# Optimization experiments

Hardware: AMD Instinct MI355X
Metric: run time of the kernel (lower is better)

## Reference

```python
import jax, jax.numpy as jnp
import numpy as np


def setup_inputs() -> dict:
    key = jax.random.key(0)
    k1, k2, k3 = jax.random.split(key, 3)
    B, idf, cdf, L, ih, iw = 16, 1024, 256, 256, 64, 64
    M = ih * iw  # 4096, conv_context2 output channels
    # scale inputs so attention logits are O(1) and softmax isn't saturated
    weightedContext = jax.random.normal(k1, (B, idf, M), dtype=jnp.float32) * 0.02
    context = jax.random.normal(k2, (B, cdf, L), dtype=jnp.float32)
    # conv1x1(cdf -> ih*iw) weight, fan-in init scale 1/sqrt(cdf)
    w2 = jax.random.normal(k3, (M, cdf), dtype=jnp.float32) * (1.0 / np.sqrt(cdf))
    return {"weightedContext": weightedContext, "context": context, "w2": w2,
            "ih": ih, "iw": iw}


def reference(weightedContext, context, w2, ih, iw):
    B = context.shape[0]
    idf = weightedContext.shape[1]
    # conv1x1 on [B, cdf, L, 1] == per-position linear: [B, ih*iw, L]
    sourceC = jnp.einsum('mc,bcl->bml', w2, context)
    # attn logits: bmm([B, idf, M], [B, M, L]) -> [B, idf, L]
    attn = jnp.einsum('bim,bml->bil', weightedContext, sourceC)
    # nn.Softmax() on [B*idf, L] view -> softmax over sourceL (last dim)
    attn = jax.nn.softmax(attn, axis=-1)
    # transpose to [B, L, idf]
    attn_c = jnp.transpose(attn, (0, 2, 1))
    # bmm([B, M, L], [B, L, idf]) -> [B, M, idf]
    wc = jnp.einsum('bml,bli->bmi', sourceC, attn_c)
    # transpose -> [B, idf, M] -> [B, idf, ih, iw]
    weightedContext_c = jnp.transpose(wc, (0, 2, 1)).reshape(B, idf, ih, iw)
    return weightedContext_c, attn_c
```

## Files before the change

### kernel.cpp

```cpp
#include <hip/hip_runtime.h>

typedef __bf16 bf16;
typedef __bf16 bf16x4 __attribute__((ext_vector_type(4)));
typedef __bf16 bf16x8 __attribute__((ext_vector_type(8)));
typedef float  f32x4  __attribute__((ext_vector_type(4)));

constexpr int NB  = 16;
constexpr int IDF = 1024;
constexpr int CDF = 256;
constexpr int L   = 256;
constexpr int M   = 4096;

__global__ __launch_bounds__(256) void k_prep_w2(const float* __restrict__ w2,
                                                 bf16* __restrict__ w2b) {
    int i = (blockIdx.x * 256 + threadIdx.x) * 4;
    float4 v = *reinterpret_cast<const float4*>(w2 + i);
    bf16x4 o; o[0] = (bf16)v.x; o[1] = (bf16)v.y; o[2] = (bf16)v.z; o[3] = (bf16)v.w;
    *reinterpret_cast<bf16x4*>(w2b + i) = o;
}

__global__ __launch_bounds__(256) void k_prep_ctxT(const float* __restrict__ ctx,
                                                   bf16* __restrict__ ctxT) {
    __shared__ float tb[32][33];
    int b = blockIdx.z, c0 = blockIdx.y * 32, l0 = blockIdx.x * 32;
    int tx = threadIdx.x, ty = threadIdx.y;
    const float* src = ctx + (size_t)b * CDF * L;
#pragma unroll
    for (int j = 0; j < 4; j++) tb[ty + 8*j][tx] = src[(size_t)(c0 + ty + 8*j) * L + l0 + tx];
    __syncthreads();
    bf16* dst = ctxT + (size_t)b * L * CDF;
#pragma unroll
    for (int j = 0; j < 4; j++) dst[(size_t)(l0 + ty + 8*j) * CDF + c0 + tx] = (bf16)tb[tx][ty + 8*j];
}

__global__ __launch_bounds__(256) void k_gemm1(const bf16* __restrict__ w2b,
                                               const bf16* __restrict__ ctxT,
                                               bf16* __restrict__ SC,
                                               bf16* __restrict__ ST) {
    __shared__ alignas(16) char smem[2 * 128 * 72 * 2];
    bf16 (*As)[72]  = reinterpret_cast<bf16(*)[72]>(smem);
    bf16 (*Bs)[72]  = reinterpret_cast<bf16(*)[72]>(smem + 128 * 72 * 2);
    bf16 (*Cs)[136] = reinterpret_cast<bf16(*)[136]>(smem);

    const int b  = blockIdx.z;
    const int m0 = blockIdx.y * 128;
    const int l0 = blockIdx.x * 128;
    const int t = threadIdx.x;
    const int lane = t & 63, wid = t >> 6;
    const int wr = (wid >> 1) * 64, wc = (wid & 1) * 64;

    const bf16* Ag = w2b + (size_t)m0 * CDF;
    const bf16* Bg = ctxT + (size_t)b * L * CDF + (size_t)l0 * CDF;

    f32x4 acc[4][4] = {};
    for (int k0 = 0; k0 < CDF; k0 += 64) {
#pragma unroll
        for (int j = 0; j < 4; j++) {
            int idx = (j * 256 + t) * 8; int r = idx >> 6, c = idx & 63;
            *reinterpret_cast<bf16x8*>(&As[r][c]) =
                *reinterpret_cast<const bf16x8*>(&Ag[(size_t)r * CDF + k0 + c]);
        }
#pragma unroll
        for (int j = 0; j < 4; j++) {
            int idx = (j * 256 + t) * 8; int r = idx >> 6, c = idx & 63;
            *reinterpret_cast<bf16x8*>(&Bs[r][c]) =
                *reinterpret_cast<const bf16x8*>(&Bg[(size_t)r * CDF + k0 + c]);
        }
        __syncthreads();
#pragma unroll
        for (int kk = 0; kk < 2; kk++) {
            const int kb = kk * 32 + (lane >> 4) * 8;
            bf16x8 af[4], bb[4];
#pragma unroll
            for (int f = 0; f < 4; f++)
                af[f] = *reinterpret_cast<const bf16x8*>(&As[wr + f * 16 + (lane & 15)][kb]);
#pragma unroll
            for (int f = 0; f < 4; f++)
                bb[f] = *reinterpret_cast<const bf16x8*>(&Bs[wc + f * 16 + (lane & 15)][kb]);
#pragma unroll
            for (int fm = 0; fm < 4; fm++)
#pragma unroll
                for (int fn = 0; fn < 4; fn++)
                    acc[fm][fn] = __builtin_amdgcn_mfma_f32_16x16x32_bf16(af[fm], bb[fn], acc[fm][fn], 0, 0, 0);
        }
        __syncthreads();
    }
#pragma unroll
    for (int fm = 0; fm < 4; fm++)
#pragma unroll
        for (int fn = 0; fn < 4; fn++) {
            int row = wr + fm * 16 + ((lane >> 4) << 2);
            int col = wc + fn * 16 + (lane & 15);
#pragma unroll
            for (int r = 0; r < 4; r++) Cs[row + r][col] = (bf16)acc[fm][fn][r];
        }
    __syncthreads();
    bf16* sc = SC + (size_t)b * M * L + (size_t)m0 * L + l0;
#pragma unroll
    for (int j = 0; j < 8; j++) {
        int idx = (j * 256 + t) * 8; int r = idx >> 7, c = idx & 127;
        *reinterpret_cast<bf16x8*>(&sc[(size_t)r * L + c]) =
            *reinterpret_cast<const bf16x8*>(&Cs[r][c]);
    }
    bf16* st = ST + (size_t)b * L * M + (size_t)l0 * M + m0;
#pragma unroll
    for (int j = 0; j < 8; j++) {
        int idx = (j * 256 + t) * 8; int lr = idx >> 7, c = idx & 127;
        bf16x8 v;
#pragma unroll
        for (int u = 0; u < 8; u++) v[u] = Cs[c + u][lr];
        *reinterpret_cast<bf16x8*>(&st[(size_t)lr * M + c]) = v;
    }
}

__global__ __launch_bounds__(256) void k_attn(const float* __restrict__ WC,
                                              const bf16* __restrict__ ST,
                                              bf16* __restrict__ AT,
                                              float* __restrict__ attn_c) {
    __shared__ alignas(16) char smem[32 * 72 * 2 + 256 * 72 * 2];
    bf16 (*As)[72] = reinterpret_cast<bf16(*)[72]>(smem);
    bf16 (*Bs)[72] = reinterpret_cast<bf16(*)[72]>(smem + 32 * 72 * 2);
    float (*Lg)[257] = reinterpret_cast<float(*)[257]>(smem);
    __shared__ float red[32][9];
    __shared__ float invbuf[32];

    const int b  = blockIdx.y;
    const int i0 = blockIdx.x * 32;
    const int t = threadIdx.x;
    const int lane = t & 63, w = t >> 6;

    const float* Ag = WC + (size_t)b * IDF * M + (size_t)i0 * M;
    const bf16*  Bg = ST + (size_t)b * L * M;

    f32x4 acc[2][4] = {};
    for (int k0 = 0; k0 < M; k0 += 64) {
#pragma unroll
        for (int j = 0; j < 2; j++) {
            int idx = (j * 256 + t) * 4; int r = idx >> 6, c = idx & 63;
            float4 v = *reinterpret_cast<const float4*>(&Ag[(size_t)r * M + k0 + c]);
            bf16x4 o; o[0] = (bf16)v.x; o[1] = (bf16)v.y; o[2] = (bf16)v.z; o[3] = (bf16)v.w;
            *reinterpret_cast<bf16x4*>(&As[r][c]) = o;
        }
#pragma unroll
        for (int j = 0; j < 8; j++) {
            int idx = (j * 256 + t) * 8; int r = idx >> 6, c = idx & 63;
            *reinterpret_cast<bf16x8*>(&Bs[r][c]) =
                *reinterpret_cast<const bf16x8*>(&Bg[(size_t)r * M + k0 + c]);
        }
        __syncthreads();
#pragma unroll
        for (int kk = 0; kk < 2; kk++) {
            const int kb = kk * 32 + (lane >> 4) * 8;
            bf16x8 af[2], bb[4];
#pragma unroll
            for (int f = 0; f < 2; f++)
                af[f] = *reinterpret_cast<const bf16x8*>(&As[f * 16 + (lane & 15)][kb]);
#pragma unroll
            for (int f = 0; f < 4; f++)
                bb[f] = *reinterpret_cast<const bf16x8*>(&Bs[w * 64 + f * 16 + (lane & 15)][kb]);
#pragma unroll
            for (int fm = 0; fm < 2; fm++)
#pragma unroll
                for (int fn = 0; fn < 4; fn++)
                    acc[fm][fn] = __builtin_amdgcn_mfma_f32_16x16x32_bf16(af[fm], bb[fn], acc[fm][fn], 0, 0, 0);
        }
        __syncthreads();
    }
#pragma unroll
    for (int fm = 0; fm < 2; fm++)
#pragma unroll
        for (int fn = 0; fn < 4; fn++) {
            int row = fm * 16 + ((lane >> 4) << 2);
            int col = w * 64 + fn * 16 + (lane & 15);
#pragma unroll
            for (int r = 0; r < 4; r++) Lg[row + r][col] = acc[fm][fn][r];
        }
    __syncthreads();
    const int srow = t & 31, sseg = t >> 5;
    float mx = -3.0e38f;
    for (int j = 0; j < 32; j++) mx = fmaxf(mx, Lg[srow][sseg * 32 + j]);
    red[srow][sseg] = mx;
    __syncthreads();
    float mrow = red[srow][0];
#pragma unroll
    for (int s = 1; s < 8; s++) mrow = fmaxf(mrow, red[srow][s]);
    __syncthreads();
    float ps = 0.f;
    for (int j = 0; j < 32; j++) {
        float e = __expf(Lg[srow][sseg * 32 + j] - mrow);
        Lg[srow][sseg * 32 + j] = e;
        ps += e;
    }
    red[srow][sseg] = ps;
    __syncthreads();
    float sum = 0.f;
#pragma unroll
    for (int s = 0; s < 8; s++) sum += red[srow][s];
    const float inv = 1.0f / sum;
    if (sseg == 0) invbuf[srow] = inv;
    __syncthreads();
    bf16* at = AT + (size_t)b * IDF * L + (size_t)i0 * L;
#pragma unroll
    for (int u = 0; u < 4; u++) {
        bf16x8 v;
#pragma unroll
        for (int q = 0; q < 8; q++) v[q] = (bf16)(Lg[srow][sseg * 32 + u * 8 + q] * inv);
        *reinterpret_cast<bf16x8*>(&at[(size_t)srow * L + sseg * 32 + u * 8]) = v;
    }
    float* ac = attn_c + (size_t)b * L * IDF + i0;
    const int i = t & 31, ls = t >> 5;
    const float invi = invbuf[i];
    for (int l = ls; l < L; l += 8)
        ac[(size_t)l * IDF + i] = Lg[i][l] * invi;
}

__global__ __launch_bounds__(256) void k_gemm3(const bf16* __restrict__ AT,
                                               const bf16* __restrict__ SC,
                                               float* __restrict__ out0) {
    __shared__ alignas(16) bf16 As[128][72];
    __shared__ alignas(16) bf16 Bs[128][72];
    const int b  = blockIdx.z;
    const int i0 = blockIdx.y * 128;
    const int m0 = blockIdx.x * 128;
    const int t = threadIdx.x;
    const int lane = t & 63, wid = t >> 6;
    const int wr = (wid >> 1) * 64, wc = (wid & 1) * 64;
    const bf16* Ag = AT + (size_t)b * IDF * L + (size_t)i0 * L;
    const bf16* Bg = SC + (size_t)b * M * L + (size_t)m0 * L;
    f32x4 acc[4][4] = {};
    for (int k0 = 0; k0 < L; k0 += 64) {
#pragma unroll
        for (int j = 0; j < 4; j++) {
            int idx = (j * 256 + t) * 8; int r = idx >> 6, c = idx & 63;
            *reinterpret_cast<bf16x8*>(&As[r][c]) =
                *reinterpret_cast<const bf16x8*>(&Ag[(size_t)r * L + k0 + c]);
        }
#pragma unroll
        for (int j = 0; j < 4; j++) {
            int idx = (j * 256 + t) * 8; int r = idx >> 6, c = idx & 63;
            *reinterpret_cast<bf16x8*>(&Bs[r][c]) =
                *reinterpret_cast<const bf16x8*>(&Bg[(size_t)r * L + k0 + c]);
        }
        __syncthreads();
#pragma unroll
        for (int kk = 0; kk < 2; kk++) {
            const int kb = kk * 32 + (lane >> 4) * 8;
            bf16x8 af[4], bb[4];
#pragma unroll
            for (int f = 0; f < 4; f++)
                af[f] = *reinterpret_cast<const bf16x8*>(&As[wr + f * 16 + (lane & 15)][kb]);
#pragma unroll
            for (int f = 0; f < 4; f++)
                bb[f] = *reinterpret_cast<const bf16x8*>(&Bs[wc + f * 16 + (lane & 15)][kb]);
#pragma unroll
            for (int fm = 0; fm < 4; fm++)
#pragma unroll
                for (int fn = 0; fn < 4; fn++)
                    acc[fm][fn] = __builtin_amdgcn_mfma_f32_16x16x32_bf16(af[fm], bb[fn], acc[fm][fn], 0, 0, 0);
        }
        __syncthreads();
    }
    float* o = out0 + (size_t)b * IDF * M + (size_t)(i0 + wr) * M + m0 + wc;
#pragma unroll
    for (int fm = 0; fm < 4; fm++)
#pragma unroll
        for (int fn = 0; fn < 4; fn++) {
            int row = fm * 16 + ((lane >> 4) << 2);
            int col = fn * 16 + (lane & 15);
#pragma unroll
            for (int r = 0; r < 4; r++) o[(size_t)(row + r) * M + col] = acc[fm][fn][r];
        }
}

extern "C" void kernel_launch(void* const* d_in, const int* in_sizes, int n_in,
                              void* d_out, int out_size, void* d_ws, size_t ws_size,
                              hipStream_t stream) {
    const float* WC  = (const float*)d_in[0];
    const float* ctx = (const float*)d_in[1];
    const float* w2  = (const float*)d_in[2];
    float* out0 = (float*)d_out;
    float* out1 = out0 + (size_t)NB * IDF * M;

    bf16* SCp  = (bf16*)d_ws;
    bf16* ATp  = SCp + (size_t)NB * M * L;
    bf16* W2B  = ATp + (size_t)NB * IDF * L;
    bf16* CTXT = W2B + (size_t)M * CDF;
    bf16* STp  = (bf16*)d_out;

    k_prep_w2 <<<dim3(M * CDF / 1024), 256, 0, stream>>>(w2, W2B);
    k_prep_ctxT<<<dim3(L / 32, CDF / 32, NB), dim3(32, 8), 0, stream>>>(ctx, CTXT);
    k_gemm1  <<<dim3(L / 128, M / 128, NB), 256, 0, stream>>>(W2B, CTXT, SCp, STp);
    k_attn   <<<dim3(IDF / 32, NB), 256, 0, stream>>>(WC, STp, ATp, out1);
    k_gemm3  <<<dim3(M / 128, IDF / 128, NB), 256, 0, stream>>>(ATp, SCp, out0);
}
```

Before: 659.4 us.

## Enlarge attention tile, use direct global-to-LDS loads with XOR swizzle, register softmax

The attention kernel now processes 64 query rows per block with 512 threads. That halves how often the ST operand is re-read relative to the WC stream. B tiles in both the attention and the final GEMM are loaded with global_load_lds into XOR-swizzled LDS instead of padded arrays, which removes register staging and bank conflicts. Softmax is computed directly from MFMA accumulators using lane shuffles plus a small cross-wave reduction, and the transposed attn_c output is written in two LDS-staged chunks as float4 stores. This cuts LDS traffic and uncoalesced stores, at the cost of larger blocks and fewer blocks in the grid.

```diff
diff --git a/kernel.cpp b/kernel.cpp
--- a/kernel.cpp
+++ b/kernel.cpp
@@ -10,6 +10,12 @@
 constexpr int CDF = 256;
 constexpr int L   = 256;
 constexpr int M   = 4096;
+
+__device__ __forceinline__ void gl_lds16(const void* g, void* l) {
+    __builtin_amdgcn_global_load_lds(
+        (const __attribute__((address_space(1))) unsigned int*)g,
+        (__attribute__((address_space(3))) unsigned int*)l, 16, 0, 0);
+}
 
 __global__ __launch_bounds__(256) void k_prep_w2(const float* __restrict__ w2,
                                                  bf16* __restrict__ w2b) {
@@ -113,51 +119,60 @@
     }
 }
 
-__global__ __launch_bounds__(256) void k_attn(const float* __restrict__ WC,
+__global__ __launch_bounds__(512) void k_attn(const float* __restrict__ WC,
                                               const bf16* __restrict__ ST,
                                               bf16* __restrict__ AT,
                                               float* __restrict__ attn_c) {
-    __shared__ alignas(16) char smem[32 * 72 * 2 + 256 * 72 * 2];
-    bf16 (*As)[72] = reinterpret_cast<bf16(*)[72]>(smem);
-    bf16 (*Bs)[72] = reinterpret_cast<bf16(*)[72]>(smem + 32 * 72 * 2);
-    float (*Lg)[257] = reinterpret_cast<float(*)[257]>(smem);
-    __shared__ float red[32][9];
-    __shared__ float invbuf[32];
+    __shared__ alignas(16) char smem[64 * 64 * 2 + 256 * 64 * 2];
+    bf16* As = reinterpret_cast<bf16*>(smem);
+    bf16* Bs = reinterpret_cast<bf16*>(smem + 8192);
+    float (*Pl)[68] = reinterpret_cast<float(*)[68]>(smem);
+    __shared__ float redm[64][4];
+    __shared__ float reds[64][4];
 
     const int b  = blockIdx.y;
-    const int i0 = blockIdx.x * 32;
-    const int t = threadIdx.x;
-    const int lane = t & 63, w = t >> 6;
+    const int i0 = blockIdx.x * 64;
+    const int t = threadIdx.x, lane = t & 63, wid = t >> 6;
+    const int wm = (wid >> 2) * 32, wn = (wid & 3) * 64;
 
     const float* Ag = WC + (size_t)b * IDF * M + (size_t)i0 * M;
     const bf16*  Bg = ST + (size_t)b * L * M;
 
+    const int arow = t >> 3;
+    const int acol = (t & 7) * 8;
+    const int aswz = (((t & 7) ^ (arow & 7)) * 8);
+    const int brow_in = lane >> 3;
+    const int bsrc = (((lane & 7) ^ brow_in) * 8);
+
     f32x4 acc[2][4] = {};
     for (int k0 = 0; k0 < M; k0 += 64) {
-#pragma unroll
-        for (int j = 0; j < 2; j++) {
-            int idx = (j * 256 + t) * 4; int r = idx >> 6, c = idx & 63;
-            float4 v = *reinterpret_cast<const float4*>(&Ag[(size_t)r * M + k0 + c]);
-            bf16x4 o; o[0] = (bf16)v.x; o[1] = (bf16)v.y; o[2] = (bf16)v.z; o[3] = (bf16)v.w;
-            *reinterpret_cast<bf16x4*>(&As[r][c]) = o;
-        }
-#pragma unroll
-        for (int j = 0; j < 8; j++) {
-            int idx = (j * 256 + t) * 8; int r = idx >> 6, c = idx & 63;
-            *reinterpret_cast<bf16x8*>(&Bs[r][c]) =
-                *reinterpret_cast<const bf16x8*>(&Bg[(size_t)r * M + k0 + c]);
+        float4 v0 = *reinterpret_cast<const float4*>(&Ag[(size_t)arow * M + k0 + acol]);
+        float4 v1 = *reinterpret_cast<const float4*>(&Ag[(size_t)arow * M + k0 + acol + 4]);
+        bf16x8 av;
+        av[0] = (bf16)v0.x; av[1] = (bf16)v0.y; av[2] = (bf16)v0.z; av[3] = (bf16)v0.w;
+        av[4] = (bf16)v1.x; av[5] = (bf16)v1.y; av[6] = (bf16)v1.z; av[7] = (bf16)v1.w;
+        *reinterpret_cast<bf16x8*>(&As[arow * 64 + aswz]) = av;
+#pragma unroll
+        for (int j = 0; j < 4; j++) {
+            int q = wid * 4 + j;
+            int row = q * 8 + brow_in;
+            gl_lds16(&Bg[(size_t)row * M + k0 + bsrc], &Bs[q * 512]);
         }
         __syncthreads();
 #pragma unroll
         for (int kk = 0; kk < 2; kk++) {
-            const int kb = kk * 32 + (lane >> 4) * 8;
+            const int g = kk * 4 + (lane >> 4);
             bf16x8 af[2], bb[4];
 #pragma unroll
-            for (int f = 0; f < 2; f++)
-                af[f] = *reinterpret_cast<const bf16x8*>(&As[f * 16 + (lane & 15)][kb]);
-#pragma unroll
-            for (int f = 0; f < 4; f++)
-                bb[f] = *reinterpret_cast<const bf16x8*>(&Bs[w * 64 + f * 16 + (lane & 15)][kb]);
+            for (int f = 0; f < 2; f++) {
+                int row = wm + f * 16 + (lane & 15);
+                af[f] = *reinterpret_cast<const bf16x8*>(&As[row * 64 + ((g ^ (row & 7)) * 8)]);
+            }
+#pragma unroll
+            for (int f = 0; f < 4; f++) {
+                int row = wn + f * 16 + (lane & 15);
+                bb[f] = *reinterpret_cast<const bf16x8*>(&Bs[row * 64 + ((g ^ (row & 7)) * 8)]);
+            }
 #pragma unroll
             for (int fm = 0; fm < 2; fm++)
 #pragma unroll
@@ -166,92 +181,127 @@
         }
         __syncthreads();
     }
+
 #pragma unroll
     for (int fm = 0; fm < 2; fm++)
 #pragma unroll
-        for (int fn = 0; fn < 4; fn++) {
-            int row = fm * 16 + ((lane >> 4) << 2);
-            int col = w * 64 + fn * 16 + (lane & 15);
-#pragma unroll
-            for (int r = 0; r < 4; r++) Lg[row + r][col] = acc[fm][fn][r];
+        for (int r = 0; r < 4; r++) {
+            float mx = fmaxf(fmaxf(acc[fm][0][r], acc[fm][1][r]),
+                             fmaxf(acc[fm][2][r], acc[fm][3][r]));
+#pragma unroll
+            for (int sh = 1; sh < 16; sh <<= 1) mx = fmaxf(mx, __shfl_xor(mx, sh));
+            if ((lane & 15) == 0)
+                redm[wm + fm * 16 + (lane >> 4) * 4 + r][wid & 3] = mx;
         }
     __syncthreads();
-    const int srow = t & 31, sseg = t >> 5;
-    float mx = -3.0e38f;
-    for (int j = 0; j < 32; j++) mx = fmaxf(mx, Lg[srow][sseg * 32 + j]);
-    red[srow][sseg] = mx;
+#pragma unroll
+    for (int fm = 0; fm < 2; fm++)
+#pragma unroll
+        for (int r = 0; r < 4; r++) {
+            int row = wm + fm * 16 + (lane >> 4) * 4 + r;
+            float mr = fmaxf(fmaxf(redm[row][0], redm[row][1]),
+                             fmaxf(redm[row][2], redm[row][3]));
+            float s = 0.f;
+#pragma unroll
+            for (int fn = 0; fn < 4; fn++) {
+                float e = __expf(acc[fm][fn][r] - mr);
+                acc[fm][fn][r] = e;
+                s += e;
+            }
+#pragma unroll
+            for (int sh = 1; sh < 16; sh <<= 1) s += __shfl_xor(s, sh);
+            if ((lane & 15) == 0) reds[row][wid & 3] = s;
+        }
     __syncthreads();
-    float mrow = red[srow][0];
-#pragma unroll
-    for (int s = 1; s < 8; s++) mrow = fmaxf(mrow, red[srow][s]);
-    __syncthreads();
-    float ps = 0.f;
-    for (int j = 0; j < 32; j++) {
-        float e = __expf(Lg[srow][sseg * 32 + j] - mrow);
-        Lg[srow][sseg * 32 + j] = e;
-        ps += e;
-    }
-    red[srow][sseg] = ps;
-    __syncthreads();
-    float sum = 0.f;
-#pragma unroll
-    for (int s = 0; s < 8; s++) sum += red[srow][s];
-    const float inv = 1.0f / sum;
-    if (sseg == 0) invbuf[srow] = inv;
-    __syncthreads();
+    float inv_[2][4];
+#pragma unroll
+    for (int fm = 0; fm < 2; fm++)
+#pragma unroll
+        for (int r = 0; r < 4; r++) {
+            int row = wm + fm * 16 + (lane >> 4) * 4 + r;
+            inv_[fm][r] = 1.0f / (reds[row][0] + reds[row][1] + reds[row][2] + reds[row][3]);
+        }
+
     bf16* at = AT + (size_t)b * IDF * L + (size_t)i0 * L;
 #pragma unroll
-    for (int u = 0; u < 4; u++) {
-        bf16x8 v;
-#pragma unroll
-        for (int q = 0; q < 8; q++) v[q] = (bf16)(Lg[srow][sseg * 32 + u * 8 + q] * inv);
-        *reinterpret_cast<bf16x8*>(&at[(size_t)srow * L + sseg * 32 + u * 8]) = v;
-    }
+    for (int fm = 0; fm < 2; fm++)
+#pragma unroll
+        for (int r = 0; r < 4; r++) {
+            int row = wm + fm * 16 + (lane >> 4) * 4 + r;
+#pragma unroll
+            for (int fn = 0; fn < 4; fn++) {
+                int col = wn + fn * 16 + (lane & 15);
+                at[(size_t)row * L + col] = (bf16)(acc[fm][fn][r] * inv_[fm][r]);
+            }
+        }
+
     float* ac = attn_c + (size_t)b * L * IDF + i0;
-    const int i = t & 31, ls = t >> 5;
-    const float invi = invbuf[i];
-    for (int l = ls; l < L; l += 8)
-        ac[(size_t)l * IDF + i] = Lg[i][l] * invi;
+#pragma unroll
+    for (int c = 0; c < 2; c++) {
+        __syncthreads();
+        if (((wid & 3) >> 1) == c) {
+#pragma unroll
+            for (int fm = 0; fm < 2; fm++)
+#pragma unroll
+                for (int r = 0; r < 4; r++) {
+                    int row = wm + fm * 16 + (lane >> 4) * 4 + r;
+                    float iv = inv_[fm][r];
+#pragma unroll
+                    for (int fn = 0; fn < 4; fn++) {
+                        int col = wn + fn * 16 + (lane & 15) - c * 128;
+                        Pl[col][row] = acc[fm][fn][r] * iv;
+                    }
+                }
+        }
+        __syncthreads();
+#pragma unroll
+        for (int s = 0; s < 4; s++) {
+            int lr = (t >> 4) + s * 32;
+            int fl = (t & 15) * 4;
+            *reinterpret_cast<float4*>(&ac[(size_t)(c * 128 + lr) * IDF + fl]) =
+                *reinterpret_cast<const float4*>(&Pl[lr][fl]);
+        }
+    }
 }
 
 __global__ __launch_bounds__(256) void k_gemm3(const bf16* __restrict__ AT,
                                                const bf16* __restrict__ SC,
                                                float* __restrict__ out0) {
-    __shared__ alignas(16) bf16 As[128][72];
-    __shared__ alignas(16) bf16 Bs[128][72];
+    __shared__ alignas(16) bf16 As[128 * 64];
+    __shared__ alignas(16) bf16 Bs[128 * 64];
     const int b  = blockIdx.z;
     const int i0 = blockIdx.y * 128;
     const int m0 = blockIdx.x * 128;
-    const int t = threadIdx.x;
-    const int lane = t & 63, wid = t >> 6;
+    const int t = threadIdx.x, lane = t & 63, wid = t >> 6;
     const int wr = (wid >> 1) * 64, wc = (wid & 1) * 64;
     const bf16* Ag = AT + (size_t)b * IDF * L + (size_t)i0 * L;
     const bf16* Bg = SC + (size_t)b * M * L + (size_t)m0 * L;
+    const int brow_in = lane >> 3;
+    const int bsrc = (((lane & 7) ^ brow_in) * 8);
     f32x4 acc[4][4] = {};
     for (int k0 = 0; k0 < L; k0 += 64) {
 #pragma unroll
         for (int j = 0; j < 4; j++) {
-            int idx = (j * 256 + t) * 8; int r = idx >> 6, c = idx & 63;
-            *reinterpret_cast<bf16x8*>(&As[r][c]) =
-                *reinterpret_cast<const bf16x8*>(&Ag[(size_t)r * L + k0 + c]);
-        }
-#pragma unroll
-        for (int j = 0; j < 4; j++) {
-            int idx = (j * 256 + t) * 8; int r = idx >> 6, c = idx & 63;
-            *reinterpret_cast<bf16x8*>(&Bs[r][c]) =
-                *reinterpret_cast<const bf16x8*>(&Bg[(size_t)r * L + k0 + c]);
+            int q = wid * 4 + j;
+            int row = q * 8 + brow_in;
+            gl_lds16(&Ag[(size_t)row * L + k0 + bsrc], &As[q * 512]);
+            gl_lds16(&Bg[(size_t)row * L + k0 + bsrc], &Bs[q * 512]);
         }
         __syncthreads();
 #pragma unroll
         for (int kk = 0; kk < 2; kk++) {
-            const int kb = kk * 32 + (lane >> 4) * 8;
+            const int g = kk * 4 + (lane >> 4);
             bf16x8 af[4], bb[4];
 #pragma unroll
-            for (int f = 0; f < 4; f++)
-                af[f] = *reinterpret_cast<const bf16x8*>(&As[wr + f * 16 + (lane & 15)][kb]);
-#pragma unroll
-            for (int f = 0; f < 4; f++)
-                bb[f] = *reinterpret_cast<const bf16x8*>(&Bs[wc + f * 16 + (lane & 15)][kb]);
+            for (int f = 0; f < 4; f++) {
+                int row = wr + f * 16 + (lane & 15);
+                af[f] = *reinterpret_cast<const bf16x8*>(&As[row * 64 + ((g ^ (row & 7)) * 8)]);
+            }
+#pragma unroll
+            for (int f = 0; f < 4; f++) {
+                int row = wc + f * 16 + (lane & 15);
+                bb[f] = *reinterpret_cast<const bf16x8*>(&Bs[row * 64 + ((g ^ (row & 7)) * 8)]);
+            }
 #pragma unroll
             for (int fm = 0; fm < 4; fm++)
 #pragma unroll
@@ -290,6 +340,6 @@
     k_prep_w2 <<<dim3(M * CDF / 1024), 256, 0, stream>>>(w2, W2B);
     k_prep_ctxT<<<dim3(L / 32, CDF / 32, NB), dim3(32, 8), 0, stream>>>(ctx, CTXT);
     k_gemm1  <<<dim3(L / 128, M / 128, NB), 256, 0, stream>>>(W2B, CTXT, SCp, STp);
-    k_attn   <<<dim3(IDF / 32, NB), 256, 0, stream>>>(WC, STp, ATp, out1);
+    k_attn   <<<dim3(IDF / 64, NB), 512, 0, stream>>>(WC, STp, ATp, out1);
     k_gemm3  <<<dim3(M / 128, IDF / 128, NB), 256, 0, stream>>>(ATp, SCp, out0);
 }
```

Result: faster. 609.0 us (-7.6%).
